# Kernel optimization log

Measured on AMD Instinct MI355X. Metric: run time of the kernel, lower is better.

The kernel has to match this reference:

```python
import jax, jax.numpy as jnp
import numpy as np

B, S = 4, 128          # batch, seq
IN, OUT = 1024, 1024   # perfect squares
C = 256                # compressed_feature_dim
K = 4                  # num_monarchs
NI, NO = 32, 32        # sqrt(IN), sqrt(OUT)
D1 = NI * NI * NO      # flat size of M1 per token
D2 = NO * NI * NO      # flat size of M2 per token


def setup_inputs() -> dict:
    key = jax.random.key(0)
    ks = jax.random.split(key, 20)
    s = 0.02
    return {
        "x":   jax.random.normal(ks[0], (B, S, IN), dtype=jnp.float32),
        # compressor: Linear(IN, C)
        "Wc":  jax.random.normal(ks[1], (IN, C), dtype=jnp.float32) * s,
        "bc":  jnp.zeros((C,), dtype=jnp.float32),
        # M1 generators (stacked over K experts): Linear(C,C), SiLU, Linear(C,D1)
        "W1a": jax.random.normal(ks[2], (K, C, C), dtype=jnp.float32) * s,
        "b1a": jnp.zeros((K, C), dtype=jnp.float32),
        "W1b": jax.random.normal(ks[3], (K, C, D1), dtype=jnp.float32) * s,
        "b1b": jax.random.normal(ks[4], (K, D1), dtype=jnp.float32) * s,
        # M2 generators
        "W2a": jax.random.normal(ks[5], (K, C, C), dtype=jnp.float32) * s,
        "b2a": jnp.zeros((K, C), dtype=jnp.float32),
        "W2b": jax.random.normal(ks[6], (K, C, D2), dtype=jnp.float32) * s,
        "b2b": jax.random.normal(ks[7], (K, D2), dtype=jnp.float32) * s,
        # mixer: Linear(C,C), SiLU, Linear(C,K)
        "Wm1": jax.random.normal(ks[8], (C, C), dtype=jnp.float32) * s,
        "bm1": jnp.zeros((C,), dtype=jnp.float32),
        "Wm2": jax.random.normal(ks[9], (C, K), dtype=jnp.float32) * s,
        "bm2": jnp.zeros((K,), dtype=jnp.float32),
        # biasor: Linear(C, OUT)
        "Wb":  jax.random.normal(ks[10], (C, OUT), dtype=jnp.float32) * s,
        "bb":  jnp.zeros((OUT,), dtype=jnp.float32),
        # ratio_gen: Linear(C, 1)
        "Wr":  jax.random.normal(ks[11], (C, 1), dtype=jnp.float32) * s,
        "br":  jnp.ones((1,), dtype=jnp.float32),
    }


def reference(x, Wc, bc, W1a, b1a, W1b, b1b, W2a, b2a, W2b, b2b,
              Wm1, bm1, Wm2, bm2, Wb, bb, Wr, br):
    silu = jax.nn.silu
    # compressor
    c = silu(x @ Wc + bc)                                   # [B,S,C]
    # per-expert hypernetwork generation of flat Monarch factors
    h1 = silu(jnp.einsum('bsc,kcd->kbsd', c, W1a) + b1a[:, None, None, :])
    M1s = jnp.einsum('kbsd,kde->kbse', h1, W1b) + b1b[:, None, None, :]  # [K,B,S,D1]
    h2 = silu(jnp.einsum('bsc,kcd->kbsd', c, W2a) + b2a[:, None, None, :])
    M2s = jnp.einsum('kbsd,kde->kbse', h2, W2b) + b2b[:, None, None, :]  # [K,B,S,D2]
    # softmax mixing coefficients
    coeffs = jax.nn.softmax(silu(c @ Wm1 + bm1) @ Wm2 + bm2, axis=-1)    # [B,S,K]
    M1_flat = jnp.einsum('kbsd,bsk->bsd', M1s, coeffs)      # [B,S,D1]
    M2_flat = jnp.einsum('kbsd,bsk->bsd', M2s, coeffs)      # [B,S,D2]
    # per-token Monarch matmul
    lead = x.shape[:-1]
    M1 = M1_flat.reshape(*lead, NI, NI, NO)
    M2 = M2_flat.reshape(*lead, NO, NI, NO)
    x1 = x.reshape(*lead, NI, NI)                            # [B,S,g=NI,i=NI]
    x1o = jnp.einsum('bsgi,bsgio->bsgo', x1, M1)             # [B,S,NI,NO]
    x2 = jnp.swapaxes(x1o, -1, -2)                           # [B,S,NO,NI]
    x2o = jnp.einsum('bsgi,bsgio->bsgo', x2, M2)             # [B,S,NO,NO]
    y = x2o.reshape(*lead, NO * NO)                          # [B,S,OUT]
    ratio = c @ Wr + br                                      # [B,S,1]
    return y * ratio + (c @ Wb + bb)
```

## Files before the change

kernel.cpp:

```cpp
#include <hip/hip_runtime.h>


typedef __bf16 bf16x8 __attribute__((ext_vector_type(8)));
typedef float  fx4    __attribute__((ext_vector_type(4)));

#define NN 32768

__device__ __forceinline__ unsigned short f2bf(float f) {
  union { float f; unsigned u; } v; v.f = f;
  unsigned r = v.u + 0x7FFFu + ((v.u >> 16) & 1u);
  return (unsigned short)(r >> 16);
}
__device__ __forceinline__ unsigned pk2(float lo, float hi) {
  return (unsigned)f2bf(lo) | ((unsigned)f2bf(hi) << 16);
}
__device__ __forceinline__ float b2f(unsigned short s) {
  union { unsigned u; float f; } v; v.u = ((unsigned)s) << 16; return v.f;
}
__device__ __forceinline__ void up8(uint4 h, float* f) {
  f[0] = b2f((unsigned short)(h.x & 0xFFFF)); f[1] = b2f((unsigned short)(h.x >> 16));
  f[2] = b2f((unsigned short)(h.y & 0xFFFF)); f[3] = b2f((unsigned short)(h.y >> 16));
  f[4] = b2f((unsigned short)(h.z & 0xFFFF)); f[5] = b2f((unsigned short)(h.z >> 16));
  f[6] = b2f((unsigned short)(h.w & 0xFFFF)); f[7] = b2f((unsigned short)(h.w >> 16));
}
__device__ __forceinline__ uint4 scale8(uint4 h, float cv) {
  uint4 u;
  u.x = pk2(b2f((unsigned short)(h.x & 0xFFFF)) * cv, b2f((unsigned short)(h.x >> 16)) * cv);
  u.y = pk2(b2f((unsigned short)(h.y & 0xFFFF)) * cv, b2f((unsigned short)(h.y >> 16)) * cv);
  u.z = pk2(b2f((unsigned short)(h.z & 0xFFFF)) * cv, b2f((unsigned short)(h.z >> 16)) * cv);
  u.w = pk2(b2f((unsigned short)(h.w & 0xFFFF)) * cv, b2f((unsigned short)(h.w >> 16)) * cv);
  return u;
}
__device__ __forceinline__ float silu_f(float x) { return x / (1.f + __expf(-x)); }

__device__ __forceinline__ void gl2lds16(const void* g, void* l) {
  __builtin_amdgcn_global_load_lds(
      (const __attribute__((address_space(1))) unsigned int*)g,
      (__attribute__((address_space(3))) unsigned int*)l, 16, 0, 0);
}

#define MFMA(a, b, c) __builtin_amdgcn_mfma_f32_16x16x32_bf16((a), (b), (c), 0, 0, 0)

__global__ __launch_bounds__(256) void k1_compress(
    const float* __restrict__ x, const float* __restrict__ Wc,
    const float* __restrict__ bc, uint4* __restrict__ c_u4) {
  const int tid = threadIdx.x;
  const int m0 = blockIdx.x * 64, n0 = blockIdx.y * 64;
  __shared__ uint4 As[8 * 64];
  __shared__ uint4 Bs[8 * 64];
  const bf16x8* Af = reinterpret_cast<const bf16x8*>(As);
  const bf16x8* Bf = reinterpret_cast<const bf16x8*>(Bs);
  uint2* Bs2 = reinterpret_cast<uint2*>(Bs);
  const int lane = tid & 63, w = tid >> 6;
  const int q = lane >> 4, rr = lane & 15;
  const int wm = (w >> 1) * 32, wn = (w & 1) * 32;
  const int bc4 = (tid & 15) * 4;
  const int brk = tid >> 4;
  const int br8 = brk & 7, bh = brk >> 3;
  fx4 a00 = 0, a01 = 0, a10 = 0, a11 = 0;

  for (int kt = 0; kt < 16; ++kt) {
    const int k0 = kt * 64;
    {
      const int run = tid & 7, mb = tid >> 3;
#pragma unroll
      for (int s = 0; s < 2; ++s) {
        const int m = mb + 32 * s;
        const float* src = x + (size_t)(m0 + m) * 1024 + k0 + run * 8;
        fx4 f0 = *(const fx4*)src;
        fx4 f1 = *(const fx4*)(src + 4);
        uint4 u; u.x = pk2(f0[0], f0[1]); u.y = pk2(f0[2], f0[3]);
        u.z = pk2(f1[0], f1[1]); u.w = pk2(f1[2], f1[3]);
        As[run * 64 + m] = u;
      }
    }
    {
      const float* bp = Wc + (size_t)(k0 + br8 * 8 + bh * 4) * 256 + n0 + bc4;
      fx4 f0 = *(const fx4*)(bp);
      fx4 f1 = *(const fx4*)(bp + 256);
      fx4 f2 = *(const fx4*)(bp + 512);
      fx4 f3 = *(const fx4*)(bp + 768);
#pragma unroll
      for (int j = 0; j < 4; ++j) {
        uint2 u; u.x = pk2(f0[j], f1[j]); u.y = pk2(f2[j], f3[j]);
        Bs2[((br8 * 64 + bc4 + j) << 1) + bh] = u;
      }
    }
    __syncthreads();
#pragma unroll
    for (int ks = 0; ks < 2; ++ks) {
      const int ro = (ks * 4 + q) * 64;
      bf16x8 fa0 = Af[ro + wm + rr];
      bf16x8 fa1 = Af[ro + wm + 16 + rr];
      bf16x8 fb0 = Bf[ro + wn + rr];
      bf16x8 fb1 = Bf[ro + wn + 16 + rr];
      a00 = MFMA(fa0, fb0, a00); a01 = MFMA(fa0, fb1, a01);
      a10 = MFMA(fa1, fb0, a10); a11 = MFMA(fa1, fb1, a11);
    }
    __syncthreads();
  }
  {
    const int r4 = tid >> 6, m = tid & 63;
    uint4 u; u.x = (r4 == 0) ? 0x3F80u : 0u; u.y = 0; u.z = 0; u.w = 0;
    As[r4 * 64 + m] = u;
    uint4 ub; ub.x = (r4 == 0) ? (unsigned)f2bf(bc[n0 + m]) : 0u;
    ub.y = 0; ub.z = 0; ub.w = 0;
    Bs[r4 * 64 + m] = ub;
  }
  __syncthreads();
  {
    const int ro = q * 64;
    bf16x8 fa0 = Af[ro + wm + rr];
    bf16x8 fa1 = Af[ro + wm + 16 + rr];
    bf16x8 fb0 = Bf[ro + wn + rr];
    bf16x8 fb1 = Bf[ro + wn + 16 + rr];
    a00 = MFMA(fa0, fb0, a00); a01 = MFMA(fa0, fb1, a01);
    a10 = MFMA(fa1, fb0, a10); a11 = MFMA(fa1, fb1, a11);
  }
  unsigned short* c16 = (unsigned short*)c_u4;
#pragma unroll
  for (int fi = 0; fi < 2; ++fi) {
#pragma unroll
    for (int fj = 0; fj < 2; ++fj) {
      fx4 v = (fi == 0) ? (fj == 0 ? a00 : a01) : (fj == 0 ? a10 : a11);
      const int cc = n0 + wn + fj * 16 + rr;
#pragma unroll
      for (int reg = 0; reg < 4; ++reg) {
        const int t = m0 + wm + fi * 16 + q * 4 + reg;
        c16[((size_t)(cc >> 3) * 512 + t) * 8 + (cc & 7)] = f2bf(silu_f(v[reg]));
      }
    }
  }
  if (blockIdx.y == 0) {
    const int r4 = tid >> 6, m = tid & 63;
    uint4 u; u.x = (r4 == 0) ? 0x3F80u : 0u; u.y = 0; u.z = 0; u.w = 0;
    c_u4[(size_t)(32 + r4) * 512 + m0 + m] = u;
  }
}

__global__ __launch_bounds__(256) void k2_hyper(
    const uint4* __restrict__ c_u4,
    const float* __restrict__ W1a, const float* __restrict__ b1a,
    const float* __restrict__ W2a, const float* __restrict__ b2a,
    const float* __restrict__ Wm1, const float* __restrict__ bm1,
    const float* __restrict__ Wb, const float* __restrict__ bb,
    unsigned short* __restrict__ H, float* __restrict__ biasout) {
  const int tid = threadIdx.x;
  const int m0 = blockIdx.x * 64, n0 = blockIdx.y * 64;
  __shared__ uint4 As[8 * 64];
  __shared__ uint4 Bs[8 * 64];
  const bf16x8* Af = reinterpret_cast<const bf16x8*>(As);
  const bf16x8* Bf = reinterpret_cast<const bf16x8*>(Bs);
  uint2* Bs2 = reinterpret_cast<uint2*>(Bs);
  const int lane = tid & 63, w = tid >> 6;
  const int q = lane >> 4, rr = lane & 15;
  const int wm = (w >> 1) * 32, wn = (w & 1) * 32;
  const int bc4 = (tid & 15) * 4;
  const int brk = tid >> 4;
  const int br8 = brk & 7, bh = brk >> 3;

  const float* bbase; const float* biasv; int bstride;
  if (n0 < 1024) {
    const int kx = n0 >> 8;
    bbase = W1a + (size_t)kx * 65536 + (n0 & 255); bstride = 256;
    biasv = b1a + kx * 256 + (n0 & 255);
  } else if (n0 < 2048) {
    const int mm = n0 - 1024; const int kx = mm >> 8;
    bbase = W2a + (size_t)kx * 65536 + (mm & 255); bstride = 256;
    biasv = b2a + kx * 256 + (mm & 255);
  } else if (n0 < 2304) {
    bbase = Wm1 + (n0 - 2048); bstride = 256; biasv = bm1 + (n0 - 2048);
  } else {
    bbase = Wb + (n0 - 2304); bstride = 1024; biasv = bb + (n0 - 2304);
  }

  fx4 a00 = 0, a01 = 0, a10 = 0, a11 = 0;
  for (int kt = 0; kt < 4; ++kt) {
#pragma unroll
    for (int s = 0; s < 2; ++s) {
      const int run = w * 2 + s;
      gl2lds16(c_u4 + (size_t)(kt * 8 + run) * 512 + m0 + lane, (void*)(As + run * 64));
    }
    {
      const float* bp = bbase + (size_t)(kt * 64 + br8 * 8 + bh * 4) * bstride + bc4;
      fx4 f0 = *(const fx4*)(bp);
      fx4 f1 = *(const fx4*)(bp + bstride);
      fx4 f2 = *(const fx4*)(bp + 2 * bstride);
      fx4 f3 = *(const fx4*)(bp + 3 * bstride);
#pragma unroll
      for (int j = 0; j < 4; ++j) {
        uint2 u; u.x = pk2(f0[j], f1[j]); u.y = pk2(f2[j], f3[j]);
        Bs2[((br8 * 64 + bc4 + j) << 1) + bh] = u;
      }
    }
    __syncthreads();
#pragma unroll
    for (int ks = 0; ks < 2; ++ks) {
      const int ro = (ks * 4 + q) * 64;
      bf16x8 fa0 = Af[ro + wm + rr];
      bf16x8 fa1 = Af[ro + wm + 16 + rr];
      bf16x8 fb0 = Bf[ro + wn + rr];
      bf16x8 fb1 = Bf[ro + wn + 16 + rr];
      a00 = MFMA(fa0, fb0, a00); a01 = MFMA(fa0, fb1, a01);
      a10 = MFMA(fa1, fb0, a10); a11 = MFMA(fa1, fb1, a11);
    }
    __syncthreads();
  }
  {
    gl2lds16(c_u4 + (size_t)(32 + w) * 512 + m0 + lane, (void*)(As + w * 64));
    const int r4 = tid >> 6, col = tid & 63;
    uint4 ub; ub.x = (r4 == 0) ? (unsigned)f2bf(biasv[col]) : 0u;
    ub.y = 0; ub.z = 0; ub.w = 0;
    Bs[r4 * 64 + col] = ub;
  }
  __syncthreads();
  {
    const int ro = q * 64;
    bf16x8 fa0 = Af[ro + wm + rr];
    bf16x8 fa1 = Af[ro + wm + 16 + rr];
    bf16x8 fb0 = Bf[ro + wn + rr];
    bf16x8 fb1 = Bf[ro + wn + 16 + rr];
    a00 = MFMA(fa0, fb0, a00); a01 = MFMA(fa0, fb1, a01);
    a10 = MFMA(fa1, fb0, a10); a11 = MFMA(fa1, fb1, a11);
  }
#pragma unroll
  for (int fi = 0; fi < 2; ++fi) {
#pragma unroll
    for (int fj = 0; fj < 2; ++fj) {
      fx4 v = (fi == 0) ? (fj == 0 ? a00 : a01) : (fj == 0 ? a10 : a11);
      const int cc = n0 + wn + fj * 16 + rr;
#pragma unroll
      for (int reg = 0; reg < 4; ++reg) {
        const int t = m0 + wm + fi * 16 + q * 4 + reg;
        if (n0 < 2304)
          H[(((size_t)(cc >> 3) * 512 + t) << 3) + (cc & 7)] = f2bf(silu_f(v[reg]));
        else
          biasout[(size_t)t * 1024 + (cc - 2304)] = v[reg];
      }
    }
  }
}

__global__ __launch_bounds__(256) void k3_prep(
    const uint4* __restrict__ Hu, const uint4* __restrict__ c_u4,
    const float* __restrict__ Wm2, const float* __restrict__ bm2,
    const float* __restrict__ Wr, const float* __restrict__ br,
    uint4* __restrict__ G1u, uint4* __restrict__ G2u, float* __restrict__ ratio) {
  const int tid = threadIdx.x;
  const int tg = blockIdx.x & 7, dgrp = blockIdx.x >> 3;
  const int t0 = tg * 64;
  __shared__ float sWm2[1024];
  __shared__ float sWr[256];
  __shared__ float part[64][4][4];
  __shared__ float rp[64][4];
  __shared__ float cf[64][4];
  ((fx4*)sWm2)[tid] = ((const fx4*)Wm2)[tid];
  if (tid < 64) ((fx4*)sWr)[tid] = ((const fx4*)Wr)[tid];
  __syncthreads();
  const int tl = tid >> 2, kx = tid & 3;
  {
    float pe0 = 0, pe1 = 0, pe2 = 0, pe3 = 0, pr = 0;
#pragma unroll
    for (int i = 0; i < 8; ++i) {
      uint4 h  = Hu[(size_t)(256 + kx * 8 + i) * 512 + t0 + tl];
      uint4 cu = c_u4[(size_t)(kx * 8 + i) * 512 + t0 + tl];
      float hf[8], cv[8];
      up8(h, hf); up8(cu, cv);
#pragma unroll
      for (int j = 0; j < 8; ++j) {
        const int ch = kx * 64 + i * 8 + j;
        pe0 += hf[j] * sWm2[ch * 4 + 0];
        pe1 += hf[j] * sWm2[ch * 4 + 1];
        pe2 += hf[j] * sWm2[ch * 4 + 2];
        pe3 += hf[j] * sWm2[ch * 4 + 3];
        pr  += cv[j] * sWr[ch];
      }
    }
    part[tl][kx][0] = pe0; part[tl][kx][1] = pe1;
    part[tl][kx][2] = pe2; part[tl][kx][3] = pe3;
    rp[tl][kx] = pr;
  }
  __syncthreads();
  if (tid < 64) {
    float l[4];
#pragma unroll
    for (int e = 0; e < 4; ++e)
      l[e] = part[tid][0][e] + part[tid][1][e] + part[tid][2][e] + part[tid][3][e] + bm2[e];
    float m = fmaxf(fmaxf(l[0], l[1]), fmaxf(l[2], l[3]));
    float e0 = __expf(l[0] - m), e1 = __expf(l[1] - m);
    float e2 = __expf(l[2] - m), e3 = __expf(l[3] - m);
    float den = e0 + e1 + e2 + e3;
    cf[tid][0] = e0 / den; cf[tid][1] = e1 / den;
    cf[tid][2] = e2 / den; cf[tid][3] = e3 / den;
    if (dgrp == 0)
      ratio[t0 + tid] = rp[tid][0] + rp[tid][1] + rp[tid][2] + rp[tid][3] + br[0];
  }
  __syncthreads();
  const int tl2 = tid & 63, sub = tid >> 6;
#pragma unroll
  for (int i = 0; i < 4; ++i) {
    const int dg = dgrp * 16 + sub * 4 + i;
    const float cv = cf[tl2][dg >> 5];
    uint4 h1 = Hu[(size_t)dg * 512 + t0 + tl2];
    G1u[(size_t)dg * 512 + t0 + tl2] = scale8(h1, cv);
    uint4 h2 = Hu[(size_t)(128 + dg) * 512 + t0 + tl2];
    G2u[(size_t)dg * 512 + t0 + tl2] = scale8(h2, cv);
  }
  if (dgrp == 0) {
    if (tid < 64) {
      uint4 u;
      u.x = pk2(cf[tid][0], cf[tid][1]);
      u.y = pk2(cf[tid][2], cf[tid][3]);
      u.z = 0; u.w = 0;
      G1u[(size_t)128 * 512 + t0 + tid] = u;
      G2u[(size_t)128 * 512 + t0 + tid] = u;
    } else {
      const int idx = tid - 64;
      uint4 z; z.x = 0; z.y = 0; z.z = 0; z.w = 0;
      G1u[(size_t)(129 + (idx >> 6)) * 512 + t0 + (idx & 63)] = z;
      G2u[(size_t)(129 + (idx >> 6)) * 512 + t0 + (idx & 63)] = z;
    }
  }
}

__global__ __launch_bounds__(256) void k_biggemm(
    const uint4* __restrict__ Gu, const float* __restrict__ W,
    const float* __restrict__ bvec, unsigned short* __restrict__ Mout) {
  const int tid = threadIdx.x;
  const int p = blockIdx.x;
  const int xcd = p & 7, slot = p >> 3;
  const int m0 = (slot & 3) * 128;
  const int n0 = ((slot >> 2) * 8 + xcd) * 128;
  __shared__ uint4 As[8 * 128];
  __shared__ uint4 Bs[8 * 128];
  const bf16x8* Af = reinterpret_cast<const bf16x8*>(As);
  const bf16x8* Bf = reinterpret_cast<const bf16x8*>(Bs);
  const int lane = tid & 63, w = tid >> 6;
  const int q = lane >> 4, rr = lane & 15;
  const int wm = (w >> 1) * 64, wn = (w & 1) * 64;
  const int colB = tid & 127, half = tid >> 7;
  const int bc4 = (tid & 31) * 4;
  const int br = tid >> 5;
  const float* wptr = W + n0 + bc4;

  fx4 acc[4][4];
#pragma unroll
  for (int i = 0; i < 4; ++i)
#pragma unroll
    for (int j = 0; j < 4; ++j) acc[i][j] = 0;

  fx4 breg[8];
#pragma unroll
  for (int kk = 0; kk < 8; ++kk)
    breg[kk] = *(const fx4*)(wptr + (size_t)(br * 8 + kk) * NN);

  for (int kt = 0; kt < 16; ++kt) {
    __syncthreads();
#pragma unroll
    for (int j = 0; j < 4; ++j) {
      uint4 u;
      u.x = pk2(breg[0][j], breg[1][j]);
      u.y = pk2(breg[2][j], breg[3][j]);
      u.z = pk2(breg[4][j], breg[5][j]);
      u.w = pk2(breg[6][j], breg[7][j]);
      Bs[br * 128 + bc4 + j] = u;
    }
#pragma unroll
    for (int s = 0; s < 4; ++s) {
      const int ch = w * 4 + s;
      const int run = ch >> 1, hf = ch & 1;
      gl2lds16(Gu + (size_t)(kt * 8 + run) * 512 + m0 + hf * 64 + lane,
               (void*)(As + run * 128 + hf * 64));
    }
    __syncthreads();
    if (kt < 15) {
#pragma unroll
      for (int kk = 0; kk < 8; ++kk)
        breg[kk] = *(const fx4*)(wptr + (size_t)((kt + 1) * 64 + br * 8 + kk) * NN);
    }
#pragma unroll
    for (int ks = 0; ks < 2; ++ks) {
      bf16x8 a[4], b[4];
      const int ro = (ks * 4 + q) * 128;
#pragma unroll
      for (int f = 0; f < 4; ++f) a[f] = Af[ro + wm + f * 16 + rr];
#pragma unroll
      for (int f = 0; f < 4; ++f) b[f] = Bf[ro + wn + f * 16 + rr];
#pragma unroll
      for (int fi = 0; fi < 4; ++fi)
#pragma unroll
        for (int fj = 0; fj < 4; ++fj) acc[fi][fj] = MFMA(a[fi], b[fj], acc[fi][fj]);
    }
  }
  __syncthreads();
#pragma unroll
  for (int s = 0; s < 2; ++s) {
    const int ch = w * 2 + s;
    const int run = ch >> 1, hf = ch & 1;
    gl2lds16(Gu + (size_t)(128 + run) * 512 + m0 + hf * 64 + lane,
             (void*)(As + run * 128 + hf * 64));
  }
  if (half == 0) {
#pragma unroll
    for (int r = 0; r < 4; ++r) {
      float v8[8];
#pragma unroll
      for (int j = 0; j < 8; ++j) {
        const int kk = r * 8 + j;
        v8[j] = (kk < 4) ? bvec[(size_t)kk * NN + n0 + colB] : 0.f;
      }
      uint4 u; u.x = pk2(v8[0], v8[1]); u.y = pk2(v8[2], v8[3]);
      u.z = pk2(v8[4], v8[5]); u.w = pk2(v8[6], v8[7]);
      Bs[r * 128 + colB] = u;
    }
  }
  __syncthreads();
  {
    bf16x8 a[4], b[4];
    const int ro = q * 128;
#pragma unroll
    for (int f = 0; f < 4; ++f) a[f] = Af[ro + wm + f * 16 + rr];
#pragma unroll
    for (int f = 0; f < 4; ++f) b[f] = Bf[ro + wn + f * 16 + rr];
#pragma unroll
    for (int fi = 0; fi < 4; ++fi)
#pragma unroll
      for (int fj = 0; fj < 4; ++fj) acc[fi][fj] = MFMA(a[fi], b[fj], acc[fi][fj]);
  }
#pragma unroll
  for (int fi = 0; fi < 4; ++fi) {
    const int tb = m0 + wm + fi * 16 + q * 4;
#pragma unroll
    for (int fj = 0; fj < 4; ++fj) {
      const fx4 v = acc[fi][fj];
      const int cc = n0 + wn + fj * 16 + rr;
#pragma unroll
      for (int reg = 0; reg < 4; ++reg)
        Mout[(size_t)(tb + reg) * NN + cc] = f2bf(v[reg]);
    }
  }
}

__global__ __launch_bounds__(256) void k_monarch1(
    const float* __restrict__ x, const unsigned short* __restrict__ M1,
    float* __restrict__ XT) {
  const int tt = blockIdx.x, tid = threadIdx.x;
  __shared__ float xs[1024];
  __shared__ float xo[1024];
  *(float4*)&xs[tid * 4] = *(const float4*)&x[(size_t)tt * 1024 + tid * 4];
  __syncthreads();
  const int g = tid >> 3, ob = (tid & 7) * 4;
  const unsigned short* mrow = M1 + (size_t)tt * NN + g * 1024 + ob;
  float a0 = 0, a1 = 0, a2 = 0, a3 = 0;
#pragma unroll
  for (int i = 0; i < 32; ++i) {
    ushort4 mv = *(const ushort4*)&mrow[i * 32];
    const float xv = xs[g * 32 + i];
    a0 += xv * b2f(mv.x); a1 += xv * b2f(mv.y);
    a2 += xv * b2f(mv.z); a3 += xv * b2f(mv.w);
  }
  xo[(ob + 0) * 32 + g] = a0; xo[(ob + 1) * 32 + g] = a1;
  xo[(ob + 2) * 32 + g] = a2; xo[(ob + 3) * 32 + g] = a3;
  __syncthreads();
  *(float4*)&XT[(size_t)tt * 1024 + tid * 4] = *(const float4*)&xo[tid * 4];
}

__global__ __launch_bounds__(256) void k_monarch2(
    const unsigned short* __restrict__ M2, const float* __restrict__ XT,
    const float* __restrict__ biasout, const float* __restrict__ ratio,
    float* __restrict__ out) {
  const int tt = blockIdx.x, tid = threadIdx.x;
  __shared__ float xs[1024];
  *(float4*)&xs[tid * 4] = *(const float4*)&XT[(size_t)tt * 1024 + tid * 4];
  __syncthreads();
  const int g = tid >> 3, ob = (tid & 7) * 4;
  const unsigned short* mrow = M2 + (size_t)tt * NN + g * 1024 + ob;
  float a0 = 0, a1 = 0, a2 = 0, a3 = 0;
#pragma unroll
  for (int i = 0; i < 32; ++i) {
    ushort4 mv = *(const ushort4*)&mrow[i * 32];
    const float xv = xs[g * 32 + i];
    a0 += xv * b2f(mv.x); a1 += xv * b2f(mv.y);
    a2 += xv * b2f(mv.z); a3 += xv * b2f(mv.w);
  }
  const float r = ratio[tt];
  float4 bo = *(const float4*)&biasout[(size_t)tt * 1024 + tid * 4];
  float4 o;
  o.x = a0 * r + bo.x; o.y = a1 * r + bo.y;
  o.z = a2 * r + bo.z; o.w = a3 * r + bo.w;
  *(float4*)&out[(size_t)tt * 1024 + tid * 4] = o;
}

extern "C" void kernel_launch(void* const* d_in, const int* in_sizes, int n_in,
                              void* d_out, int out_size, void* d_ws, size_t ws_size,
                              hipStream_t stream) {
  (void)in_sizes; (void)n_in; (void)out_size; (void)ws_size;
  const float* x   = (const float*)d_in[0];
  const float* Wc  = (const float*)d_in[1];
  const float* bc  = (const float*)d_in[2];
  const float* W1a = (const float*)d_in[3];
  const float* b1a = (const float*)d_in[4];
  const float* W1b = (const float*)d_in[5];
  const float* b1b = (const float*)d_in[6];
  const float* W2a = (const float*)d_in[7];
  const float* b2a = (const float*)d_in[8];
  const float* W2b = (const float*)d_in[9];
  const float* b2b = (const float*)d_in[10];
  const float* Wm1 = (const float*)d_in[11];
  const float* bm1 = (const float*)d_in[12];
  const float* Wm2 = (const float*)d_in[13];
  const float* bm2 = (const float*)d_in[14];
  const float* Wb  = (const float*)d_in[15];
  const float* bb  = (const float*)d_in[16];
  const float* Wr  = (const float*)d_in[17];
  const float* br  = (const float*)d_in[18];
  float* out = (float*)d_out;

  char* ws = (char*)d_ws;
  uint4* c_u4            = (uint4*)(ws + 0);
  unsigned short* H      = (unsigned short*)(ws + 294912);
  float* biasout         = (float*)(ws + 2654208);
  uint4* G1u             = (uint4*)(ws + 4751360);
  uint4* G2u             = (uint4*)(ws + 5832704);
  float* ratio           = (float*)(ws + 6914048);
  float* XT              = (float*)(ws + 6918144);
  unsigned short* M      = (unsigned short*)(ws + 9015296);

  k1_compress<<<dim3(8, 4), 256, 0, stream>>>(x, Wc, bc, c_u4);
  k2_hyper<<<dim3(8, 52), 256, 0, stream>>>(c_u4, W1a, b1a, W2a, b2a, Wm1, bm1,
                                            Wb, bb, H, biasout);
  k3_prep<<<64, 256, 0, stream>>>((const uint4*)H, c_u4, Wm2, bm2, Wr, br,
                                  G1u, G2u, ratio);
  k_biggemm<<<1024, 256, 0, stream>>>(G1u, W1b, b1b, M);
  k_monarch1<<<512, 256, 0, stream>>>(x, M, XT);
  k_biggemm<<<1024, 256, 0, stream>>>(G2u, W2b, b2b, M);
  k_monarch2<<<512, 256, 0, stream>>>(M, XT, biasout, ratio, out);
}
```

Baseline: 472.9 us.

## Prefetch GEMM operands, pad LDS, permute Monarch output layout for wide loads

The compress and hyper GEMMs now prefetch the next K-tile into registers, and the A tile is double-buffered through async global-to-LDS loads, so global latency overlaps with MFMA work. The B tile gets a padded LDS row stride to reduce bank conflicts. The big GEMM writes the generated Monarch factors in a permuted column order. The Monarch kernels then process two tokens per block with 16-byte loads that cover 8 contiguous outputs. This trades more LDS and register use for fewer barriers, better coalescing and lower load latency, and the new index math adds some risk of layout mistakes.

```diff
diff --git a/kernel.cpp b/kernel.cpp
--- a/kernel.cpp
+++ b/kernel.cpp
@@ -47,73 +47,85 @@
   const int tid = threadIdx.x;
   const int m0 = blockIdx.x * 64, n0 = blockIdx.y * 64;
   __shared__ uint4 As[8 * 64];
-  __shared__ uint4 Bs[8 * 64];
+  __shared__ uint4 Bs[8 * 65];
   const bf16x8* Af = reinterpret_cast<const bf16x8*>(As);
   const bf16x8* Bf = reinterpret_cast<const bf16x8*>(Bs);
   uint2* Bs2 = reinterpret_cast<uint2*>(Bs);
   const int lane = tid & 63, w = tid >> 6;
   const int q = lane >> 4, rr = lane & 15;
   const int wm = (w >> 1) * 32, wn = (w & 1) * 32;
-  const int bc4 = (tid & 15) * 4;
-  const int brk = tid >> 4;
-  const int br8 = brk & 7, bh = brk >> 3;
+  const int arun = tid & 7, amb = tid >> 3;
+  const int kgrp = tid & 15, colg = tid >> 4;
   fx4 a00 = 0, a01 = 0, a10 = 0, a11 = 0;
+  fx4 areg[4], breg[4];
+
+#pragma unroll
+  for (int s = 0; s < 2; ++s) {
+    const float* src = x + (size_t)(m0 + amb + 32 * s) * 1024 + arun * 8;
+    areg[2 * s] = *(const fx4*)src;
+    areg[2 * s + 1] = *(const fx4*)(src + 4);
+  }
+#pragma unroll
+  for (int kk = 0; kk < 4; ++kk)
+    breg[kk] = *(const fx4*)(Wc + (size_t)(kgrp * 4 + kk) * 256 + n0 + colg * 4);
 
   for (int kt = 0; kt < 16; ++kt) {
-    const int k0 = kt * 64;
-    {
-      const int run = tid & 7, mb = tid >> 3;
+    __syncthreads();
+#pragma unroll
+    for (int s = 0; s < 2; ++s) {
+      uint4 u;
+      u.x = pk2(areg[2 * s][0], areg[2 * s][1]);
+      u.y = pk2(areg[2 * s][2], areg[2 * s][3]);
+      u.z = pk2(areg[2 * s + 1][0], areg[2 * s + 1][1]);
+      u.w = pk2(areg[2 * s + 1][2], areg[2 * s + 1][3]);
+      As[arun * 64 + amb + 32 * s] = u;
+    }
+#pragma unroll
+    for (int j = 0; j < 4; ++j) {
+      uint2 u;
+      u.x = pk2(breg[0][j], breg[1][j]);
+      u.y = pk2(breg[2][j], breg[3][j]);
+      Bs2[(((kgrp >> 1) * 65 + colg * 4 + j) << 1) + (kgrp & 1)] = u;
+    }
+    __syncthreads();
+    if (kt < 15) {
+      const int k0 = (kt + 1) * 64;
 #pragma unroll
       for (int s = 0; s < 2; ++s) {
-        const int m = mb + 32 * s;
-        const float* src = x + (size_t)(m0 + m) * 1024 + k0 + run * 8;
-        fx4 f0 = *(const fx4*)src;
-        fx4 f1 = *(const fx4*)(src + 4);
-        uint4 u; u.x = pk2(f0[0], f0[1]); u.y = pk2(f0[2], f0[3]);
-        u.z = pk2(f1[0], f1[1]); u.w = pk2(f1[2], f1[3]);
-        As[run * 64 + m] = u;
-      }
-    }
-    {
-      const float* bp = Wc + (size_t)(k0 + br8 * 8 + bh * 4) * 256 + n0 + bc4;
-      fx4 f0 = *(const fx4*)(bp);
-      fx4 f1 = *(const fx4*)(bp + 256);
-      fx4 f2 = *(const fx4*)(bp + 512);
-      fx4 f3 = *(const fx4*)(bp + 768);
-#pragma unroll
-      for (int j = 0; j < 4; ++j) {
-        uint2 u; u.x = pk2(f0[j], f1[j]); u.y = pk2(f2[j], f3[j]);
-        Bs2[((br8 * 64 + bc4 + j) << 1) + bh] = u;
-      }
-    }
-    __syncthreads();
+        const float* src = x + (size_t)(m0 + amb + 32 * s) * 1024 + k0 + arun * 8;
+        areg[2 * s] = *(const fx4*)src;
+        areg[2 * s + 1] = *(const fx4*)(src + 4);
+      }
+#pragma unroll
+      for (int kk = 0; kk < 4; ++kk)
+        breg[kk] = *(const fx4*)(Wc + (size_t)(k0 + kgrp * 4 + kk) * 256 + n0 + colg * 4);
+    }
 #pragma unroll
     for (int ks = 0; ks < 2; ++ks) {
-      const int ro = (ks * 4 + q) * 64;
-      bf16x8 fa0 = Af[ro + wm + rr];
-      bf16x8 fa1 = Af[ro + wm + 16 + rr];
-      bf16x8 fb0 = Bf[ro + wn + rr];
-      bf16x8 fb1 = Bf[ro + wn + 16 + rr];
+      const int roA = (ks * 4 + q) * 64, roB = (ks * 4 + q) * 65;
+      bf16x8 fa0 = Af[roA + wm + rr];
+      bf16x8 fa1 = Af[roA + wm + 16 + rr];
+      bf16x8 fb0 = Bf[roB + wn + rr];
+      bf16x8 fb1 = Bf[roB + wn + 16 + rr];
       a00 = MFMA(fa0, fb0, a00); a01 = MFMA(fa0, fb1, a01);
       a10 = MFMA(fa1, fb0, a10); a11 = MFMA(fa1, fb1, a11);
     }
-    __syncthreads();
-  }
+  }
+  __syncthreads();
   {
     const int r4 = tid >> 6, m = tid & 63;
     uint4 u; u.x = (r4 == 0) ? 0x3F80u : 0u; u.y = 0; u.z = 0; u.w = 0;
     As[r4 * 64 + m] = u;
     uint4 ub; ub.x = (r4 == 0) ? (unsigned)f2bf(bc[n0 + m]) : 0u;
     ub.y = 0; ub.z = 0; ub.w = 0;
-    Bs[r4 * 64 + m] = ub;
-  }
-  __syncthreads();
-  {
-    const int ro = q * 64;
-    bf16x8 fa0 = Af[ro + wm + rr];
-    bf16x8 fa1 = Af[ro + wm + 16 + rr];
-    bf16x8 fb0 = Bf[ro + wn + rr];
-    bf16x8 fb1 = Bf[ro + wn + 16 + rr];
+    Bs[r4 * 65 + m] = ub;
+  }
+  __syncthreads();
+  {
+    bf16x8 fa0 = Af[q * 64 + wm + rr];
+    bf16x8 fa1 = Af[q * 64 + wm + 16 + rr];
+    bf16x8 fb0 = Bf[q * 65 + wn + rr];
+    bf16x8 fb1 = Bf[q * 65 + wn + 16 + rr];
     a00 = MFMA(fa0, fb0, a00); a01 = MFMA(fa0, fb1, a01);
     a10 = MFMA(fa1, fb0, a10); a11 = MFMA(fa1, fb1, a11);
   }
@@ -147,17 +159,14 @@
     unsigned short* __restrict__ H, float* __restrict__ biasout) {
   const int tid = threadIdx.x;
   const int m0 = blockIdx.x * 64, n0 = blockIdx.y * 64;
-  __shared__ uint4 As[8 * 64];
-  __shared__ uint4 Bs[8 * 64];
-  const bf16x8* Af = reinterpret_cast<const bf16x8*>(As);
+  __shared__ uint4 As[2][8 * 64];
+  __shared__ uint4 Bs[8 * 65];
   const bf16x8* Bf = reinterpret_cast<const bf16x8*>(Bs);
   uint2* Bs2 = reinterpret_cast<uint2*>(Bs);
   const int lane = tid & 63, w = tid >> 6;
   const int q = lane >> 4, rr = lane & 15;
   const int wm = (w >> 1) * 32, wn = (w & 1) * 32;
-  const int bc4 = (tid & 15) * 4;
-  const int brk = tid >> 4;
-  const int br8 = brk & 7, bh = brk >> 3;
+  const int kgrp = tid & 15, colg = tid >> 4;
 
   const float* bbase; const float* biasv; int bstride;
   if (n0 < 1024) {
@@ -175,51 +184,65 @@
   }
 
   fx4 a00 = 0, a01 = 0, a10 = 0, a11 = 0;
+  fx4 breg[4];
+#pragma unroll
+  for (int kk = 0; kk < 4; ++kk)
+    breg[kk] = *(const fx4*)(bbase + (size_t)(kgrp * 4 + kk) * bstride + colg * 4);
+#pragma unroll
+  for (int s = 0; s < 2; ++s) {
+    const int run = w * 2 + s;
+    gl2lds16(c_u4 + (size_t)run * 512 + m0 + lane, (void*)(&As[0][run * 64]));
+  }
+  int cur = 0;
   for (int kt = 0; kt < 4; ++kt) {
-#pragma unroll
-    for (int s = 0; s < 2; ++s) {
-      const int run = w * 2 + s;
-      gl2lds16(c_u4 + (size_t)(kt * 8 + run) * 512 + m0 + lane, (void*)(As + run * 64));
-    }
-    {
-      const float* bp = bbase + (size_t)(kt * 64 + br8 * 8 + bh * 4) * bstride + bc4;
-      fx4 f0 = *(const fx4*)(bp);
-      fx4 f1 = *(const fx4*)(bp + bstride);
-      fx4 f2 = *(const fx4*)(bp + 2 * bstride);
-      fx4 f3 = *(const fx4*)(bp + 3 * bstride);
-#pragma unroll
-      for (int j = 0; j < 4; ++j) {
-        uint2 u; u.x = pk2(f0[j], f1[j]); u.y = pk2(f2[j], f3[j]);
-        Bs2[((br8 * 64 + bc4 + j) << 1) + bh] = u;
-      }
-    }
     __syncthreads();
 #pragma unroll
+    for (int j = 0; j < 4; ++j) {
+      uint2 u;
+      u.x = pk2(breg[0][j], breg[1][j]);
+      u.y = pk2(breg[2][j], breg[3][j]);
+      Bs2[(((kgrp >> 1) * 65 + colg * 4 + j) << 1) + (kgrp & 1)] = u;
+    }
+    __syncthreads();
+    if (kt < 3) {
+#pragma unroll
+      for (int s = 0; s < 2; ++s) {
+        const int run = w * 2 + s;
+        gl2lds16(c_u4 + (size_t)((kt + 1) * 8 + run) * 512 + m0 + lane,
+                 (void*)(&As[cur ^ 1][run * 64]));
+      }
+#pragma unroll
+      for (int kk = 0; kk < 4; ++kk)
+        breg[kk] = *(const fx4*)(bbase + (size_t)((kt + 1) * 64 + kgrp * 4 + kk) * bstride + colg * 4);
+    }
+    const bf16x8* Af = reinterpret_cast<const bf16x8*>(As[cur]);
+#pragma unroll
     for (int ks = 0; ks < 2; ++ks) {
-      const int ro = (ks * 4 + q) * 64;
-      bf16x8 fa0 = Af[ro + wm + rr];
-      bf16x8 fa1 = Af[ro + wm + 16 + rr];
-      bf16x8 fb0 = Bf[ro + wn + rr];
-      bf16x8 fb1 = Bf[ro + wn + 16 + rr];
+      const int roA = (ks * 4 + q) * 64, roB = (ks * 4 + q) * 65;
+      bf16x8 fa0 = Af[roA + wm + rr];
+      bf16x8 fa1 = Af[roA + wm + 16 + rr];
+      bf16x8 fb0 = Bf[roB + wn + rr];
+      bf16x8 fb1 = Bf[roB + wn + 16 + rr];
       a00 = MFMA(fa0, fb0, a00); a01 = MFMA(fa0, fb1, a01);
       a10 = MFMA(fa1, fb0, a10); a11 = MFMA(fa1, fb1, a11);
     }
-    __syncthreads();
-  }
-  {
-    gl2lds16(c_u4 + (size_t)(32 + w) * 512 + m0 + lane, (void*)(As + w * 64));
+    cur ^= 1;
+  }
+  __syncthreads();
+  {
+    gl2lds16(c_u4 + (size_t)(32 + w) * 512 + m0 + lane, (void*)(&As[0][w * 64]));
     const int r4 = tid >> 6, col = tid & 63;
     uint4 ub; ub.x = (r4 == 0) ? (unsigned)f2bf(biasv[col]) : 0u;
     ub.y = 0; ub.z = 0; ub.w = 0;
-    Bs[r4 * 64 + col] = ub;
-  }
-  __syncthreads();
-  {
-    const int ro = q * 64;
-    bf16x8 fa0 = Af[ro + wm + rr];
-    bf16x8 fa1 = Af[ro + wm + 16 + rr];
-    bf16x8 fb0 = Bf[ro + wn + rr];
-    bf16x8 fb1 = Bf[ro + wn + 16 + rr];
+    Bs[r4 * 65 + col] = ub;
+  }
+  __syncthreads();
+  {
+    const bf16x8* Af = reinterpret_cast<const bf16x8*>(As[0]);
+    bf16x8 fa0 = Af[q * 64 + wm + rr];
+    bf16x8 fa1 = Af[q * 64 + wm + 16 + rr];
+    bf16x8 fb0 = Bf[q * 65 + wn + rr];
+    bf16x8 fb1 = Bf[q * 65 + wn + 16 + rr];
     a00 = MFMA(fa0, fb0, a00); a01 = MFMA(fa0, fb1, a01);
     a10 = MFMA(fa1, fb0, a10); a11 = MFMA(fa1, fb1, a11);
   }
@@ -331,17 +354,16 @@
   const int xcd = p & 7, slot = p >> 3;
   const int m0 = (slot & 3) * 128;
   const int n0 = ((slot >> 2) * 8 + xcd) * 128;
-  __shared__ uint4 As[8 * 128];
-  __shared__ uint4 Bs[8 * 128];
-  const bf16x8* Af = reinterpret_cast<const bf16x8*>(As);
+  __shared__ uint4 As[2][8 * 128];
+  __shared__ uint4 Bs[8 * 129];
   const bf16x8* Bf = reinterpret_cast<const bf16x8*>(Bs);
   const int lane = tid & 63, w = tid >> 6;
   const int q = lane >> 4, rr = lane & 15;
   const int wm = (w >> 1) * 64, wn = (w & 1) * 64;
   const int colB = tid & 127, half = tid >> 7;
-  const int bc4 = (tid & 31) * 4;
-  const int br = tid >> 5;
-  const float* wptr = W + n0 + bc4;
+  const int bcg = tid >> 3;
+  const int br  = tid & 7;
+  const float* wptr = W + n0 + bcg * 4;
 
   fx4 acc[4][4];
 #pragma unroll
@@ -353,7 +375,14 @@
 #pragma unroll
   for (int kk = 0; kk < 8; ++kk)
     breg[kk] = *(const fx4*)(wptr + (size_t)(br * 8 + kk) * NN);
-
+#pragma unroll
+  for (int s = 0; s < 4; ++s) {
+    const int ch = w * 4 + s, run = ch >> 1, hf = ch & 1;
+    gl2lds16(Gu + (size_t)run * 512 + m0 + hf * 64 + lane,
+             (void*)(&As[0][run * 128 + hf * 64]));
+  }
+
+  int cur = 0;
   for (int kt = 0; kt < 16; ++kt) {
     __syncthreads();
 #pragma unroll
@@ -363,42 +392,42 @@
       u.y = pk2(breg[2][j], breg[3][j]);
       u.z = pk2(breg[4][j], breg[5][j]);
       u.w = pk2(breg[6][j], breg[7][j]);
-      Bs[br * 128 + bc4 + j] = u;
-    }
-#pragma unroll
-    for (int s = 0; s < 4; ++s) {
-      const int ch = w * 4 + s;
-      const int run = ch >> 1, hf = ch & 1;
-      gl2lds16(Gu + (size_t)(kt * 8 + run) * 512 + m0 + hf * 64 + lane,
-               (void*)(As + run * 128 + hf * 64));
+      Bs[br * 129 + bcg * 4 + j] = u;
     }
     __syncthreads();
     if (kt < 15) {
 #pragma unroll
+      for (int s = 0; s < 4; ++s) {
+        const int ch = w * 4 + s, run = ch >> 1, hf = ch & 1;
+        gl2lds16(Gu + (size_t)((kt + 1) * 8 + run) * 512 + m0 + hf * 64 + lane,
+                 (void*)(&As[cur ^ 1][run * 128 + hf * 64]));
+      }
+#pragma unroll
       for (int kk = 0; kk < 8; ++kk)
         breg[kk] = *(const fx4*)(wptr + (size_t)((kt + 1) * 64 + br * 8 + kk) * NN);
     }
+    const bf16x8* Afc = reinterpret_cast<const bf16x8*>(As[cur]);
 #pragma unroll
     for (int ks = 0; ks < 2; ++ks) {
       bf16x8 a[4], b[4];
-      const int ro = (ks * 4 + q) * 128;
-#pragma unroll
-      for (int f = 0; f < 4; ++f) a[f] = Af[ro + wm + f * 16 + rr];
-#pragma unroll
-      for (int f = 0; f < 4; ++f) b[f] = Bf[ro + wn + f * 16 + rr];
+      const int roA = (ks * 4 + q) * 128, roB = (ks * 4 + q) * 129;
+#pragma unroll
+      for (int f = 0; f < 4; ++f) a[f] = Afc[roA + wm + f * 16 + rr];
+#pragma unroll
+      for (int f = 0; f < 4; ++f) b[f] = Bf[roB + wn + f * 16 + rr];
 #pragma unroll
       for (int fi = 0; fi < 4; ++fi)
 #pragma unroll
         for (int fj = 0; fj < 4; ++fj) acc[fi][fj] = MFMA(a[fi], b[fj], acc[fi][fj]);
     }
+    cur ^= 1;
   }
   __syncthreads();
 #pragma unroll
   for (int s = 0; s < 2; ++s) {
-    const int ch = w * 2 + s;
-    const int run = ch >> 1, hf = ch & 1;
+    const int ch = w * 2 + s, run = ch >> 1, hf = ch & 1;
     gl2lds16(Gu + (size_t)(128 + run) * 512 + m0 + hf * 64 + lane,
-             (void*)(As + run * 128 + hf * 64));
+             (void*)(&As[0][run * 128 + hf * 64]));
   }
   if (half == 0) {
 #pragma unroll
@@ -411,17 +440,17 @@
       }
       uint4 u; u.x = pk2(v8[0], v8[1]); u.y = pk2(v8[2], v8[3]);
       u.z = pk2(v8[4], v8[5]); u.w = pk2(v8[6], v8[7]);
-      Bs[r * 128 + colB] = u;
-    }
-  }
-  __syncthreads();
-  {
+      Bs[r * 129 + colB] = u;
+    }
+  }
+  __syncthreads();
+  {
+    const bf16x8* Af0 = reinterpret_cast<const bf16x8*>(As[0]);
     bf16x8 a[4], b[4];
-    const int ro = q * 128;
-#pragma unroll
-    for (int f = 0; f < 4; ++f) a[f] = Af[ro + wm + f * 16 + rr];
-#pragma unroll
-    for (int f = 0; f < 4; ++f) b[f] = Bf[ro + wn + f * 16 + rr];
+#pragma unroll
+    for (int f = 0; f < 4; ++f) a[f] = Af0[q * 128 + wm + f * 16 + rr];
+#pragma unroll
+    for (int f = 0; f < 4; ++f) b[f] = Bf[q * 129 + wn + f * 16 + rr];
 #pragma unroll
     for (int fi = 0; fi < 4; ++fi)
 #pragma unroll
@@ -434,61 +463,85 @@
     for (int fj = 0; fj < 4; ++fj) {
       const fx4 v = acc[fi][fj];
       const int cc = n0 + wn + fj * 16 + rr;
+      const int pc = ((cc >> 5) & 31) * 1024 + (cc >> 10) * 32 + (cc & 31);
 #pragma unroll
       for (int reg = 0; reg < 4; ++reg)
-        Mout[(size_t)(tb + reg) * NN + cc] = f2bf(v[reg]);
+        Mout[(size_t)(tb + reg) * NN + pc] = f2bf(v[reg]);
     }
   }
 }
 
 __global__ __launch_bounds__(256) void k_monarch1(
-    const float* __restrict__ x, const unsigned short* __restrict__ M1,
+    const float* __restrict__ x, const unsigned short* __restrict__ M1p,
     float* __restrict__ XT) {
-  const int tt = blockIdx.x, tid = threadIdx.x;
-  __shared__ float xs[1024];
-  __shared__ float xo[1024];
-  *(float4*)&xs[tid * 4] = *(const float4*)&x[(size_t)tt * 1024 + tid * 4];
-  __syncthreads();
-  const int g = tid >> 3, ob = (tid & 7) * 4;
-  const unsigned short* mrow = M1 + (size_t)tt * NN + g * 1024 + ob;
-  float a0 = 0, a1 = 0, a2 = 0, a3 = 0;
+  const int tp = blockIdx.x, tid = threadIdx.x;
+  const int tl = tid >> 7, t2 = tid & 127;
+  const int tt = tp * 2 + tl;
+  __shared__ float xs[2][1024];
+  __shared__ float xo[2][1024];
+  {
+    const int base = tid * 8;
+    *(float4*)&(((float*)xs)[base])     = *(const float4*)&x[(size_t)tp * 2048 + base];
+    *(float4*)&(((float*)xs)[base + 4]) = *(const float4*)&x[(size_t)tp * 2048 + base + 4];
+  }
+  __syncthreads();
+  const int g = t2 >> 2, ob = (t2 & 3) * 8;
+  const unsigned short* mrow = M1p + (size_t)tt * NN + g * 32 + ob;
+  float acc[8] = {0, 0, 0, 0, 0, 0, 0, 0};
 #pragma unroll
   for (int i = 0; i < 32; ++i) {
-    ushort4 mv = *(const ushort4*)&mrow[i * 32];
-    const float xv = xs[g * 32 + i];
-    a0 += xv * b2f(mv.x); a1 += xv * b2f(mv.y);
-    a2 += xv * b2f(mv.z); a3 += xv * b2f(mv.w);
-  }
-  xo[(ob + 0) * 32 + g] = a0; xo[(ob + 1) * 32 + g] = a1;
-  xo[(ob + 2) * 32 + g] = a2; xo[(ob + 3) * 32 + g] = a3;
-  __syncthreads();
-  *(float4*)&XT[(size_t)tt * 1024 + tid * 4] = *(const float4*)&xo[tid * 4];
+    uint4 mv = *(const uint4*)&mrow[(size_t)i * 1024];
+    float mf[8]; up8(mv, mf);
+    const float xv = xs[tl][g * 32 + i];
+#pragma unroll
+    for (int j = 0; j < 8; ++j) acc[j] += xv * mf[j];
+  }
+#pragma unroll
+  for (int j = 0; j < 8; ++j) xo[tl][(ob + j) * 32 + g] = acc[j];
+  __syncthreads();
+  {
+    const int base = tid * 8;
+    *(float4*)&XT[(size_t)tp * 2048 + base]     = *(const float4*)&(((float*)xo)[base]);
+    *(float4*)&XT[(size_t)tp * 2048 + base + 4] = *(const float4*)&(((float*)xo)[base + 4]);
+  }
 }
 
 __global__ __launch_bounds__(256) void k_monarch2(
-    const unsigned short* __restrict__ M2, const float* __restrict__ XT,
+    const unsigned short* __restrict__ M2p, const float* __restrict__ XT,
     const float* __restrict__ biasout, const float* __restrict__ ratio,
     float* __restrict__ out) {
-  const int tt = blockIdx.x, tid = threadIdx.x;
-  __shared__ float xs[1024];
-  *(float4*)&xs[tid * 4] = *(const float4*)&XT[(size_t)tt * 1024 + tid * 4];
-  __syncthreads();
-  const int g = tid >> 3, ob = (tid & 7) * 4;
-  const unsigned short* mrow = M2 + (size_t)tt * NN + g * 1024 + ob;
-  float a0 = 0, a1 = 0, a2 = 0, a3 = 0;
+  const int tp = blockIdx.x, tid = threadIdx.x;
+  const int tl = tid >> 7, t2 = tid & 127;
+  const int tt = tp * 2 + tl;
+  __shared__ float xs[2][1024];
+  {
+    const int base = tid * 8;
+    *(float4*)&(((float*)xs)[base])     = *(const float4*)&XT[(size_t)tp * 2048 + base];
+    *(float4*)&(((float*)xs)[base + 4]) = *(const float4*)&XT[(size_t)tp * 2048 + base + 4];
+  }
+  __syncthreads();
+  const int g = t2 >> 2, ob = (t2 & 3) * 8;
+  const unsigned short* mrow = M2p + (size_t)tt * NN + g * 32 + ob;
+  float acc[8] = {0, 0, 0, 0, 0, 0, 0, 0};
 #pragma unroll
   for (int i = 0; i < 32; ++i) {
-    ushort4 mv = *(const ushort4*)&mrow[i * 32];
-    const float xv = xs[g * 32 + i];
-    a0 += xv * b2f(mv.x); a1 += xv * b2f(mv.y);
-    a2 += xv * b2f(mv.z); a3 += xv * b2f(mv.w);
+    uint4 mv = *(const uint4*)&mrow[(size_t)i * 1024];
+    float mf[8]; up8(mv, mf);
+    const float xv = xs[tl][g * 32 + i];
+#pragma unroll
+    for (int j = 0; j < 8; ++j) acc[j] += xv * mf[j];
   }
   const float r = ratio[tt];
-  float4 bo = *(const float4*)&biasout[(size_t)tt * 1024 + tid * 4];
-  float4 o;
-  o.x = a0 * r + bo.x; o.y = a1 * r + bo.y;
-  o.z = a2 * r + bo.z; o.w = a3 * r + bo.w;
-  *(float4*)&out[(size_t)tt * 1024 + tid * 4] = o;
+  const int col = g * 32 + ob;
+  float4 b0 = *(const float4*)&biasout[(size_t)tt * 1024 + col];
+  float4 b1 = *(const float4*)&biasout[(size_t)tt * 1024 + col + 4];
+  float4 o0, o1;
+  o0.x = acc[0] * r + b0.x; o0.y = acc[1] * r + b0.y;
+  o0.z = acc[2] * r + b0.z; o0.w = acc[3] * r + b0.w;
+  o1.x = acc[4] * r + b1.x; o1.y = acc[5] * r + b1.y;
+  o1.z = acc[6] * r + b1.z; o1.w = acc[7] * r + b1.w;
+  *(float4*)&out[(size_t)tt * 1024 + col]     = o0;
+  *(float4*)&out[(size_t)tt * 1024 + col + 4] = o1;
 }
 
 extern "C" void kernel_launch(void* const* d_in, const int* in_sizes, int n_in,
@@ -532,7 +585,7 @@
   k3_prep<<<64, 256, 0, stream>>>((const uint4*)H, c_u4, Wm2, bm2, Wr, br,
                                   G1u, G2u, ratio);
   k_biggemm<<<1024, 256, 0, stream>>>(G1u, W1b, b1b, M);
-  k_monarch1<<<512, 256, 0, stream>>>(x, M, XT);
+  k_monarch1<<<256, 256, 0, stream>>>(x, M, XT);
   k_biggemm<<<1024, 256, 0, stream>>>(G2u, W2b, b2b, M);
-  k_monarch2<<<512, 256, 0, stream>>>(M, XT, biasout, ratio, out);
-}
+  k_monarch2<<<256, 256, 0, stream>>>(M, XT, biasout, ratio, out);
+}
```

After: 501.4 us. 1.06x slower.
